# Performance work log

Measured on AMD Instinct MI355X. Metric: run time of the kernel, lower is better.

The kernel has to match this reference:

```python
import jax, jax.numpy as jnp
from jax import lax
import numpy as np

B, T, A = 128, 2048, 3
H = 100  # LSTM units
F = 64   # conv filters


def setup_inputs() -> dict:
    key = jax.random.key(0)
    ks = jax.random.split(key, 8)
    s = lambda k, shape, scale: (jax.random.normal(k, shape, dtype=jnp.float32) * scale)
    return {
        "state_input": s(ks[0], (B, T, 1), 1.0),
        "conv_w": s(ks[1], (2, 1, F), 0.5),
        "conv_b": jnp.zeros((F,), jnp.float32),
        "lstm1_w": s(ks[2], (F, 4 * H), 0.08),
        "lstm1_u": s(ks[3], (H, 4 * H), 0.08),
        "lstm1_b": jnp.zeros((4 * H,), jnp.float32),
        "lstm2_w": s(ks[4], (H, 4 * H), 0.08),
        "lstm2_u": s(ks[5], (H, 4 * H), 0.08),
        "lstm2_b": jnp.zeros((4 * H,), jnp.float32),
        "dense_w": s(ks[6], (H, A), 0.1),
        "dense_b": jnp.zeros((A,), jnp.float32),
    }


def _lstm_relu(x, W, U, b, return_sequences):
    # Keras LSTM with activation='relu', recurrent_activation='sigmoid'.
    # Gate order: i, f, g(candidate), o. h = o * relu(c).
    Bz = x.shape[0]
    xz = jnp.einsum("btf,fg->btg", x, W) + b  # precompute input projections [B,T,4H]
    h0 = jnp.zeros((Bz, U.shape[0]), x.dtype)
    c0 = jnp.zeros_like(h0)

    def step(carry, xz_t):
        h, c = carry
        z = xz_t + h @ U
        i, f, g, o = jnp.split(z, 4, axis=-1)
        i = jax.nn.sigmoid(i)
        f = jax.nn.sigmoid(f)
        g = jax.nn.relu(g)
        o = jax.nn.sigmoid(o)
        c = f * c + i * g
        h = o * jax.nn.relu(c)
        return (h, c), (h if return_sequences else 0.0)

    (h_last, _), hs = lax.scan(step, (h0, c0), jnp.swapaxes(xz, 0, 1))
    if return_sequences:
        return jnp.swapaxes(hs, 0, 1)  # [B,T,H]
    return h_last


def reference(state_input, conv_w, conv_b, lstm1_w, lstm1_u, lstm1_b,
              lstm2_w, lstm2_u, lstm2_b, dense_w, dense_b):
    # Conv1D(filters=64, kernel_size=2, padding='valid', relu): [B,T,1]->[B,T-1,64]
    x = lax.conv_general_dilated(
        state_input, conv_w, window_strides=(1,), padding="VALID",
        dimension_numbers=("NWC", "WIO", "NWC"))
    x = jax.nn.relu(x + conv_b)
    # MaxPool1D(pool_size=1) is the identity.
    x = _lstm_relu(x, lstm1_w, lstm1_u, lstm1_b, return_sequences=True)
    # Dropout at inference is identity.
    x = _lstm_relu(x, lstm2_w, lstm2_u, lstm2_b, return_sequences=False)  # [B,H]
    logits = x @ dense_w + dense_b
    return jax.nn.softmax(logits, axis=-1)
```

## Files before the change

### kernel.cpp

```cpp
#include <hip/hip_runtime.h>
#include <math.h>


typedef _Float16 h2 __attribute__((ext_vector_type(2)));

#define TT 2048
#define TP 2047
#define HH 100
#define G4 400
#define FF 64
#define NB 128

#define X1R 176
#define CBQ 104
#define NPW (400 * 88)
#define NCW (400 * 100)
#define CHK 64
#define NCHUNK 32
#define RINGC 4
#define CHUNK_DW (CHK * 50)

#define WS_FLAGS (NPW + NCW)
#define WS_RING  (WS_FLAGS + 256)

#define FD2(w, xs, acc) acc = __builtin_amdgcn_fdot2(w, xs, acc, false)
#define B2(f) __builtin_bit_cast(h2, f)

static __device__ __forceinline__ float psum2(float z) {
    int p = __builtin_amdgcn_update_dpp(0, __builtin_bit_cast(int, z),
                                        0xB1, 0xF, 0xF, true);
    return z + __builtin_bit_cast(float, p);
}
static __device__ __forceinline__ float xswap2(float z) {
    int p = __builtin_amdgcn_update_dpp(0, __builtin_bit_cast(int, z),
                                        0x4E, 0xF, 0xF, true);
    return __builtin_bit_cast(float, p);
}
static __device__ __forceinline__ float sig(float z) {
    return 1.0f / (1.0f + __expf(-z));
}
static __device__ __forceinline__ void step_barrier() {
    __builtin_amdgcn_sched_barrier(0);
    asm volatile("s_waitcnt lgkmcnt(0)" ::: "memory");
    __builtin_amdgcn_sched_barrier(0);
    __builtin_amdgcn_s_barrier();
    __builtin_amdgcn_sched_barrier(0);
}

__global__ void prep_weights(const float* __restrict__ w1, const float* __restrict__ u1,
                             const float* __restrict__ w2, const float* __restrict__ u2,
                             h2* __restrict__ ws)
{
    const int idx = blockIdx.x * 256 + threadIdx.x;
    if (idx >= NPW + NCW) return;
    float lo = 0.f, hi = 0.f;
    if (idx < NPW) {
        const int rt = idx / 88, r = idx % 88;
        const int qq = (r >> 2) * 2 + ((r & 3) >> 1);
        const int gs = r & 1;
        const int p = rt >> 2, g2 = (rt >> 1) & 1, kh = rt & 1;
        const int col = (2 * g2 + gs) * HH + p;
        const int E0 = 2 * qq;
#pragma unroll
        for (int e = 0; e < 2; ++e) {
            const int E = E0 + e;
            float v = 0.f;
            if (E < 82) {
                const int k = kh * 82 + E;
                v = (k < FF) ? w1[k * G4 + col] : u1[(k - FF) * G4 + col];
            }
            if (e == 0) lo = v; else hi = v;
        }
    } else {
        const int i2 = idx - NPW;
        const int rt = i2 / 100, r = i2 % 100;
        const int qq = (r >> 2) * 2 + ((r & 3) >> 1);
        const int gs = r & 1;
        const int p = rt >> 2, g2 = (rt >> 1) & 1, kh = rt & 1;
        const int col = (2 * g2 + gs) * HH + p;
        const int k0 = 2 * qq;
        const float* M = kh ? u2 : w2;
        lo = M[k0 * G4 + col];
        hi = M[(k0 + 1) * G4 + col];
    }
    ws[idx] = h2{(_Float16)lo, (_Float16)hi};
}

__global__ __launch_bounds__(448, 1)
void fused_lstm_kernel(const float* __restrict__ s,
                       const float* __restrict__ conv_w,
                       const float* __restrict__ conv_b,
                       const float* __restrict__ b1,
                       const float* __restrict__ b2,
                       const float* __restrict__ dw, const float* __restrict__ db,
                       h2* __restrict__ wpk,
                       float* __restrict__ out)
{
    const int tid  = threadIdx.x;
    const int bb   = blockIdx.x;
    const int b    = bb & (NB - 1);
    const bool prod = bb < NB;

    int* pflag = (int*)(wpk + WS_FLAGS) + b;
    int* aflag = (int*)(wpk + WS_FLAGS) + 128 + b;
    unsigned* ring = (unsigned*)(wpk + WS_RING) + (size_t)b * (RINGC * CHUNK_DW);

    __shared__ float s_buf[TT];
    __shared__ __align__(16) _Float16 X1[2 * X1R];
    __shared__ __align__(16) _Float16 CB[CHK * CBQ];
    __shared__ __align__(16) _Float16 HR[2 * CBQ];

    if (prod) {
        for (int i = tid; i < TT; i += 448) s_buf[i] = s[(size_t)b * TT + i];
        if (tid < X1R) ((unsigned*)X1)[tid] = 0u;
    } else {
        if (tid < CBQ) ((unsigned*)HR)[tid] = 0u;
        if (tid < CHK * 2)
            ((unsigned*)CB)[(tid >> 1) * 52 + 50 + (tid & 1)] = 0u;
    }
    __syncthreads();

    if (prod) {
        const int rt = tid;
        const int active = rt < 400;
        const int lrt = active ? rt : 0;
        const int p  = lrt >> 2;
        const int g2 = (lrt >> 1) & 1;
        const int kh = lrt & 1;
        const int cL = (2 * g2) * HH + p;

        h2 wa[44], wb[44];
        {
            const float4* w4 = (const float4*)(wpk + (size_t)lrt * 88);
#pragma unroll
            for (int j = 0; j < 22; ++j) {
                const float4 v = w4[j];
                wa[2*j]   = B2(v.x); wb[2*j]   = B2(v.y);
                wa[2*j+1] = B2(v.z); wb[2*j+1] = B2(v.w);
            }
        }
        const float bL = b1[cL], bH = b1[cL + HH];
        const int hoff = (p < 18) ? (64 + p) : (p + 70);

        const int f1 = rt - 400;
        float cv0 = 0.f, cv1 = 0.f, cb0 = 0.f, cv0b = 0.f, cv1b = 0.f, cb0b = 0.f;
        if (!active) {
            cv0 = conv_w[f1]; cv1 = conv_w[FF + f1]; cb0 = conv_b[f1];
            if (f1 < 16) { cv0b = conv_w[48 + f1]; cv1b = conv_w[FF + 48 + f1]; cb0b = conv_b[48 + f1]; }
        }
        if (!active) {
            X1[f1] = (_Float16)fmaxf(fmaf(s_buf[0], cv0, fmaf(s_buf[1], cv1, cb0)), 0.f);
            if (f1 < 16)
                X1[48 + f1] = (_Float16)fmaxf(fmaf(s_buf[0], cv0b, fmaf(s_buf[1], cv1b, cb0b)), 0.f);
        }
        __syncthreads();

        float c = 0.0f;
        for (int t = 0; t < TP; ++t) {
            if ((t & 63) == 0) {
                const int k = t >> 6;
                if (tid == 0 && k >= RINGC) {
                    int g = 0;
                    while (__hip_atomic_load(aflag, __ATOMIC_ACQUIRE,
                                             __HIP_MEMORY_SCOPE_AGENT) < k - (RINGC - 1)
                           && g < 50000000) { ++g; __builtin_amdgcn_s_sleep(8); }
                }
                __syncthreads();
            }
            if (active) {
                _Float16* cur = X1 + (t & 1) * X1R;
                _Float16* nx1 = X1 + ((t & 1) ^ 1) * X1R;
                float za0 = 0.f, za1 = 0.f, zb0 = 0.f, zb1 = 0.f;
                const float4* vb = (const float4*)(cur + kh * 88);
#pragma unroll
                for (int r2 = 0; r2 < 11; ++r2) {
                    const float4 v = vb[r2];
                    FD2(wa[4*r2+0], B2(v.x), za0); FD2(wb[4*r2+0], B2(v.x), zb0);
                    FD2(wa[4*r2+1], B2(v.y), za1); FD2(wb[4*r2+1], B2(v.y), zb1);
                    FD2(wa[4*r2+2], B2(v.z), za0); FD2(wb[4*r2+2], B2(v.z), zb0);
                    FD2(wa[4*r2+3], B2(v.w), za1); FD2(wb[4*r2+3], B2(v.w), zb1);
                }
                const float zaS = psum2(za0 + za1) + bL;
                const float zbS = psum2(zb0 + zb1) + bH;
                const float oa = xswap2(zaS), ob = xswap2(zbS);
                const float zi = g2 ? oa  : zaS;
                const float zf = g2 ? ob  : zbS;
                const float zg = g2 ? zaS : oa;
                const float zo = g2 ? zbS : ob;
                c = fmaf(sig(zf), c, sig(zi) * fmaxf(zg, 0.f));
                const float h = sig(zo) * fmaxf(c, 0.f);
                if ((rt & 3) == 0) {
                    const _Float16 hq = (_Float16)h;
                    nx1[hoff] = hq;
                    const unsigned hb = (unsigned)__builtin_bit_cast(unsigned short, hq);
                    const unsigned prt =
                        (unsigned)__builtin_amdgcn_ds_swizzle((int)hb, 0x101F) & 0xFFFFu;
                    if (!(p & 1))
                        __hip_atomic_store(ring + ((t >> 6) & 3) * CHUNK_DW
                                                + (t & 63) * 50 + (p >> 1),
                                           hb | (prt << 16), __ATOMIC_RELAXED,
                                           __HIP_MEMORY_SCOPE_AGENT);
                }
                if (((t & 63) == 63) || (t == TP - 1))
                    asm volatile("s_waitcnt vmcnt(0)" ::: "memory");
            } else if (t + 1 < TP) {
                _Float16* nx1 = X1 + ((t & 1) ^ 1) * X1R;
                nx1[f1] = (_Float16)fmaxf(
                    fmaf(s_buf[t + 1], cv0, fmaf(s_buf[t + 2], cv1, cb0)), 0.f);
                if (f1 < 16)
                    nx1[48 + f1] = (_Float16)fmaxf(
                        fmaf(s_buf[t + 1], cv0b, fmaf(s_buf[t + 2], cv1b, cb0b)), 0.f);
            }
            step_barrier();
            if (tid == 0 && (((t & 63) == 63) || (t == TP - 1)))
                __hip_atomic_fetch_add(pflag, 1, __ATOMIC_RELEASE,
                                       __HIP_MEMORY_SCOPE_AGENT);
        }
    } else {
        const int rt = tid;
        const int active = rt < 400;
        const int lrt = active ? rt : 0;
        const int p  = lrt >> 2;
        const int g2 = (lrt >> 1) & 1;
        const int kh = lrt & 1;
        const int cL = (2 * g2) * HH + p;

        h2 wa[50], wb[50];
        {
            const float4* w4 = (const float4*)(wpk + NPW + (size_t)lrt * 100);
#pragma unroll
            for (int j = 0; j < 25; ++j) {
                const float4 v = w4[j];
                wa[2*j]   = B2(v.x); wb[2*j]   = B2(v.y);
                wa[2*j+1] = B2(v.z); wb[2*j+1] = B2(v.w);
            }
        }
        const float bL = b2[cL], bH = b2[cL + HH];
        __syncthreads();

        float c = 0.0f;
        for (int k = 0; k < NCHUNK; ++k) {
            if (tid == 0) {
                int g = 0;
                while (__hip_atomic_load(pflag, __ATOMIC_ACQUIRE,
                                         __HIP_MEMORY_SCOPE_AGENT) < k + 1
                       && g < 50000000) { ++g; __builtin_amdgcn_s_sleep(8); }
            }
            __syncthreads();
            const int csz = (TP - (k << 6) < CHK) ? (TP - (k << 6)) : CHK;
            unsigned* gsrc = ring + (k & 3) * CHUNK_DW;
            for (int d = tid; d < csz * 50; d += 448)
                ((unsigned*)CB)[(d / 50) * 52 + (d % 50)] =
                    __hip_atomic_load(gsrc + d, __ATOMIC_RELAXED,
                                      __HIP_MEMORY_SCOPE_AGENT);
            __syncthreads();
            if (tid == 0)
                __hip_atomic_fetch_add(aflag, 1, __ATOMIC_RELAXED,
                                       __HIP_MEMORY_SCOPE_AGENT);
            for (int lt = 0; lt < csz; ++lt) {
                const int t = (k << 6) + lt;
                if (active) {
                    const _Float16* base = kh ? (HR + (t & 1) * CBQ)
                                              : (CB + lt * CBQ);
                    float za0 = 0.f, za1 = 0.f, zb0 = 0.f, zb1 = 0.f;
                    const float4* vb = (const float4*)base;
#pragma unroll
                    for (int r2 = 0; r2 < 12; ++r2) {
                        const float4 v = vb[r2];
                        FD2(wa[4*r2+0], B2(v.x), za0); FD2(wb[4*r2+0], B2(v.x), zb0);
                        FD2(wa[4*r2+1], B2(v.y), za1); FD2(wb[4*r2+1], B2(v.y), zb1);
                        FD2(wa[4*r2+2], B2(v.z), za0); FD2(wb[4*r2+2], B2(v.z), zb0);
                        FD2(wa[4*r2+3], B2(v.w), za1); FD2(wb[4*r2+3], B2(v.w), zb1);
                    }
                    {
                        const float2 tv = *(const float2*)(base + 96);
                        FD2(wa[48], B2(tv.x), za0); FD2(wb[48], B2(tv.x), zb0);
                        FD2(wa[49], B2(tv.y), za1); FD2(wb[49], B2(tv.y), zb1);
                    }
                    const float zaS = psum2(za0 + za1) + bL;
                    const float zbS = psum2(zb0 + zb1) + bH;
                    const float oa = xswap2(zaS), ob = xswap2(zbS);
                    const float zi = g2 ? oa  : zaS;
                    const float zf = g2 ? ob  : zbS;
                    const float zg = g2 ? zaS : oa;
                    const float zo = g2 ? zbS : ob;
                    c = fmaf(sig(zf), c, sig(zi) * fmaxf(zg, 0.f));
                    const float h = sig(zo) * fmaxf(c, 0.f);
                    if ((rt & 3) == 0)
                        HR[((t & 1) ^ 1) * CBQ + p] = (_Float16)h;
                }
                step_barrier();
            }
        }

        if (rt == 0) {
            float l[3];
#pragma unroll
            for (int a = 0; a < 3; ++a) {
                float acc = db[a];
                for (int j = 0; j < HH; ++j)
                    acc = fmaf((float)HR[CBQ + j], dw[j * 3 + a], acc);
                l[a] = acc;
            }
            const float m = fmaxf(l[0], fmaxf(l[1], l[2]));
            const float e0 = __expf(l[0] - m), e1 = __expf(l[1] - m), e2 = __expf(l[2] - m);
            const float inv = 1.0f / (e0 + e1 + e2);
            out[b * 3 + 0] = e0 * inv;
            out[b * 3 + 1] = e1 * inv;
            out[b * 3 + 2] = e2 * inv;
        }
    }
}

extern "C" void kernel_launch(void* const* d_in, const int* in_sizes, int n_in,
                              void* d_out, int out_size, void* d_ws, size_t ws_size,
                              hipStream_t stream) {
    const float* s      = (const float*)d_in[0];
    const float* conv_w = (const float*)d_in[1];
    const float* conv_b = (const float*)d_in[2];
    const float* w1     = (const float*)d_in[3];
    const float* u1     = (const float*)d_in[4];
    const float* b1     = (const float*)d_in[5];
    const float* w2     = (const float*)d_in[6];
    const float* u2     = (const float*)d_in[7];
    const float* b2     = (const float*)d_in[8];
    const float* dw     = (const float*)d_in[9];
    const float* db     = (const float*)d_in[10];

    h2* ws = (h2*)d_ws;
    hipMemsetAsync((void*)((int*)(ws + WS_FLAGS)), 0, 256 * sizeof(int), stream);
    const int nh2 = NPW + NCW;
    prep_weights<<<(nh2 + 255) / 256, 256, 0, stream>>>(w1, u1, w2, u2, ws);
    fused_lstm_kernel<<<256, 448, 0, stream>>>(
        s, conv_w, conv_b, b1, b2, dw, db, ws, (float*)d_out);
}
```

Measured before the change: 2.063 ms.

## Halve threads per LSTM step by dropping the K-split reduction across lane pairs

Each gate pair is now computed by one thread over the full input dimension instead of being split across two threads, which removes the DPP pair-sum and reduces the block from 448 to 256 threads. Weights are repacked so each thread holds twice as many fp16 pairs in registers, and the conv lanes, h placement and swizzle pattern are adjusted to match. The aim is fewer waves per block and a cheaper cross-lane step on the serial recurrence, in exchange for a longer dependent dot-product chain and more register pressure per thread.

New measurement: 2.156 ms. 4.5% more time.

```diff
diff --git a/kernel.cpp b/kernel.cpp
--- a/kernel.cpp
+++ b/kernel.cpp
@@ -11,10 +11,10 @@
 #define FF 64
 #define NB 128
 
-#define X1R 176
+#define X1R 168
 #define CBQ 104
-#define NPW (400 * 88)
-#define NCW (400 * 100)
+#define NPW (200 * 164)
+#define NCW (200 * 200)
 #define CHK 64
 #define NCHUNK 32
 #define RINGC 4
@@ -26,14 +26,9 @@
 #define FD2(w, xs, acc) acc = __builtin_amdgcn_fdot2(w, xs, acc, false)
 #define B2(f) __builtin_bit_cast(h2, f)
 
-static __device__ __forceinline__ float psum2(float z) {
+static __device__ __forceinline__ float xswap1(float z) {
     int p = __builtin_amdgcn_update_dpp(0, __builtin_bit_cast(int, z),
                                         0xB1, 0xF, 0xF, true);
-    return z + __builtin_bit_cast(float, p);
-}
-static __device__ __forceinline__ float xswap2(float z) {
-    int p = __builtin_amdgcn_update_dpp(0, __builtin_bit_cast(int, z),
-                                        0x4E, 0xF, 0xF, true);
     return __builtin_bit_cast(float, p);
 }
 static __device__ __forceinline__ float sig(float z) {
@@ -55,38 +50,72 @@
     if (idx >= NPW + NCW) return;
     float lo = 0.f, hi = 0.f;
     if (idx < NPW) {
-        const int rt = idx / 88, r = idx % 88;
+        const int rt = idx / 164, r = idx % 164;
         const int qq = (r >> 2) * 2 + ((r & 3) >> 1);
         const int gs = r & 1;
-        const int p = rt >> 2, g2 = (rt >> 1) & 1, kh = rt & 1;
+        const int p = rt >> 1, g2 = rt & 1;
         const int col = (2 * g2 + gs) * HH + p;
-        const int E0 = 2 * qq;
+        const int k0 = 2 * qq;
 #pragma unroll
         for (int e = 0; e < 2; ++e) {
-            const int E = E0 + e;
-            float v = 0.f;
-            if (E < 82) {
-                const int k = kh * 82 + E;
-                v = (k < FF) ? w1[k * G4 + col] : u1[(k - FF) * G4 + col];
-            }
+            const int k = k0 + e;
+            const float v = (k < FF) ? w1[k * G4 + col] : u1[(k - FF) * G4 + col];
             if (e == 0) lo = v; else hi = v;
         }
     } else {
         const int i2 = idx - NPW;
-        const int rt = i2 / 100, r = i2 % 100;
+        const int rt = i2 / 200, r = i2 % 200;
         const int qq = (r >> 2) * 2 + ((r & 3) >> 1);
         const int gs = r & 1;
-        const int p = rt >> 2, g2 = (rt >> 1) & 1, kh = rt & 1;
+        const int p = rt >> 1, g2 = rt & 1;
         const int col = (2 * g2 + gs) * HH + p;
         const int k0 = 2 * qq;
-        const float* M = kh ? u2 : w2;
-        lo = M[k0 * G4 + col];
-        hi = M[(k0 + 1) * G4 + col];
+#pragma unroll
+        for (int e = 0; e < 2; ++e) {
+            const int k = k0 + e;
+            const float v = (k < HH) ? w2[k * G4 + col] : u2[(k - HH) * G4 + col];
+            if (e == 0) lo = v; else hi = v;
+        }
     }
     ws[idx] = h2{(_Float16)lo, (_Float16)hi};
 }
 
-__global__ __launch_bounds__(448, 1)
+#define PDOTF(base) { const float4* vb = (const float4*)(base); \
+_Pragma("unroll") \
+    for (int r2 = 0; r2 < 20; ++r2) { \
+        const float4 v = vb[r2]; \
+        FD2(wa[4*r2+0], B2(v.x), za0); FD2(wb[4*r2+0], B2(v.x), zb0); \
+        FD2(wa[4*r2+1], B2(v.y), za1); FD2(wb[4*r2+1], B2(v.y), zb1); \
+        FD2(wa[4*r2+2], B2(v.z), za0); FD2(wb[4*r2+2], B2(v.z), zb0); \
+        FD2(wa[4*r2+3], B2(v.w), za1); FD2(wb[4*r2+3], B2(v.w), zb1); \
+    } \
+    { const float2 tv = *(const float2*)((base) + 160); \
+      FD2(wa[80], B2(tv.x), za0); FD2(wb[80], B2(tv.x), zb0); \
+      FD2(wa[81], B2(tv.y), za1); FD2(wb[81], B2(tv.y), zb1); } }
+
+#define CDOTH(base, WO) { const float4* vb = (const float4*)(base); \
+_Pragma("unroll") \
+    for (int r2 = 0; r2 < 12; ++r2) { \
+        const float4 v = vb[r2]; \
+        FD2(wa[(WO)+4*r2+0], B2(v.x), za0); FD2(wb[(WO)+4*r2+0], B2(v.x), zb0); \
+        FD2(wa[(WO)+4*r2+1], B2(v.y), za1); FD2(wb[(WO)+4*r2+1], B2(v.y), zb1); \
+        FD2(wa[(WO)+4*r2+2], B2(v.z), za0); FD2(wb[(WO)+4*r2+2], B2(v.z), zb0); \
+        FD2(wa[(WO)+4*r2+3], B2(v.w), za1); FD2(wb[(WO)+4*r2+3], B2(v.w), zb1); \
+    } \
+    { const float2 tv = *(const float2*)((base) + 96); \
+      FD2(wa[(WO)+48], B2(tv.x), za0); FD2(wb[(WO)+48], B2(tv.x), zb0); \
+      FD2(wa[(WO)+49], B2(tv.y), za1); FD2(wb[(WO)+49], B2(tv.y), zb1); } }
+
+#define GCELL1(zaS, zbS, cc, hh_) { \
+    const float oa = xswap1(zaS), ob = xswap1(zbS); \
+    const float zi = g2 ? oa  : zaS; \
+    const float zf = g2 ? ob  : zbS; \
+    const float zg = g2 ? zaS : oa; \
+    const float zo = g2 ? zbS : ob; \
+    cc = fmaf(sig(zf), cc, sig(zi) * fmaxf(zg, 0.f)); \
+    hh_ = sig(zo) * fmaxf(cc, 0.f); }
+
+__global__ __launch_bounds__(256, 1)
 void fused_lstm_kernel(const float* __restrict__ s,
                        const float* __restrict__ conv_w,
                        const float* __restrict__ conv_b,
@@ -111,7 +140,7 @@
     __shared__ __align__(16) _Float16 HR[2 * CBQ];
 
     if (prod) {
-        for (int i = tid; i < TT; i += 448) s_buf[i] = s[(size_t)b * TT + i];
+        for (int i = tid; i < TT; i += 256) s_buf[i] = s[(size_t)b * TT + i];
         if (tid < X1R) ((unsigned*)X1)[tid] = 0u;
     } else {
         if (tid < CBQ) ((unsigned*)HR)[tid] = 0u;
@@ -122,36 +151,34 @@
 
     if (prod) {
         const int rt = tid;
-        const int active = rt < 400;
+        const int active = rt < 200;
         const int lrt = active ? rt : 0;
-        const int p  = lrt >> 2;
-        const int g2 = (lrt >> 1) & 1;
-        const int kh = lrt & 1;
+        const int p  = lrt >> 1;
+        const int g2 = lrt & 1;
         const int cL = (2 * g2) * HH + p;
 
-        h2 wa[44], wb[44];
+        h2 wa[82], wb[82];
         {
-            const float4* w4 = (const float4*)(wpk + (size_t)lrt * 88);
-#pragma unroll
-            for (int j = 0; j < 22; ++j) {
+            const float4* w4 = (const float4*)(wpk + (size_t)lrt * 164);
+#pragma unroll
+            for (int j = 0; j < 41; ++j) {
                 const float4 v = w4[j];
                 wa[2*j]   = B2(v.x); wb[2*j]   = B2(v.y);
                 wa[2*j+1] = B2(v.z); wb[2*j+1] = B2(v.w);
             }
         }
         const float bL = b1[cL], bH = b1[cL + HH];
-        const int hoff = (p < 18) ? (64 + p) : (p + 70);
-
-        const int f1 = rt - 400;
+
+        const int f1 = rt - 200;
         float cv0 = 0.f, cv1 = 0.f, cb0 = 0.f, cv0b = 0.f, cv1b = 0.f, cb0b = 0.f;
         if (!active) {
             cv0 = conv_w[f1]; cv1 = conv_w[FF + f1]; cb0 = conv_b[f1];
-            if (f1 < 16) { cv0b = conv_w[48 + f1]; cv1b = conv_w[FF + 48 + f1]; cb0b = conv_b[48 + f1]; }
+            if (f1 < 8) { cv0b = conv_w[56 + f1]; cv1b = conv_w[FF + 56 + f1]; cb0b = conv_b[56 + f1]; }
         }
         if (!active) {
             X1[f1] = (_Float16)fmaxf(fmaf(s_buf[0], cv0, fmaf(s_buf[1], cv1, cb0)), 0.f);
-            if (f1 < 16)
-                X1[48 + f1] = (_Float16)fmaxf(fmaf(s_buf[0], cv0b, fmaf(s_buf[1], cv1b, cb0b)), 0.f);
+            if (f1 < 8)
+                X1[56 + f1] = (_Float16)fmaxf(fmaf(s_buf[0], cv0b, fmaf(s_buf[1], cv1b, cb0b)), 0.f);
         }
         __syncthreads();
 
@@ -171,30 +198,17 @@
                 _Float16* cur = X1 + (t & 1) * X1R;
                 _Float16* nx1 = X1 + ((t & 1) ^ 1) * X1R;
                 float za0 = 0.f, za1 = 0.f, zb0 = 0.f, zb1 = 0.f;
-                const float4* vb = (const float4*)(cur + kh * 88);
-#pragma unroll
-                for (int r2 = 0; r2 < 11; ++r2) {
-                    const float4 v = vb[r2];
-                    FD2(wa[4*r2+0], B2(v.x), za0); FD2(wb[4*r2+0], B2(v.x), zb0);
-                    FD2(wa[4*r2+1], B2(v.y), za1); FD2(wb[4*r2+1], B2(v.y), zb1);
-                    FD2(wa[4*r2+2], B2(v.z), za0); FD2(wb[4*r2+2], B2(v.z), zb0);
-                    FD2(wa[4*r2+3], B2(v.w), za1); FD2(wb[4*r2+3], B2(v.w), zb1);
-                }
-                const float zaS = psum2(za0 + za1) + bL;
-                const float zbS = psum2(zb0 + zb1) + bH;
-                const float oa = xswap2(zaS), ob = xswap2(zbS);
-                const float zi = g2 ? oa  : zaS;
-                const float zf = g2 ? ob  : zbS;
-                const float zg = g2 ? zaS : oa;
-                const float zo = g2 ? zbS : ob;
-                c = fmaf(sig(zf), c, sig(zi) * fmaxf(zg, 0.f));
-                const float h = sig(zo) * fmaxf(c, 0.f);
-                if ((rt & 3) == 0) {
+                PDOTF(cur)
+                const float zaS = za0 + za1 + bL;
+                const float zbS = zb0 + zb1 + bH;
+                float h;
+                GCELL1(zaS, zbS, c, h)
+                if (!g2) {
                     const _Float16 hq = (_Float16)h;
-                    nx1[hoff] = hq;
+                    nx1[FF + p] = hq;
                     const unsigned hb = (unsigned)__builtin_bit_cast(unsigned short, hq);
                     const unsigned prt =
-                        (unsigned)__builtin_amdgcn_ds_swizzle((int)hb, 0x101F) & 0xFFFFu;
+                        (unsigned)__builtin_amdgcn_ds_swizzle((int)hb, 0x081F) & 0xFFFFu;
                     if (!(p & 1))
                         __hip_atomic_store(ring + ((t >> 6) & 3) * CHUNK_DW
                                                 + (t & 63) * 50 + (p >> 1),
@@ -207,8 +221,8 @@
                 _Float16* nx1 = X1 + ((t & 1) ^ 1) * X1R;
                 nx1[f1] = (_Float16)fmaxf(
                     fmaf(s_buf[t + 1], cv0, fmaf(s_buf[t + 2], cv1, cb0)), 0.f);
-                if (f1 < 16)
-                    nx1[48 + f1] = (_Float16)fmaxf(
+                if (f1 < 8)
+                    nx1[56 + f1] = (_Float16)fmaxf(
                         fmaf(s_buf[t + 1], cv0b, fmaf(s_buf[t + 2], cv1b, cb0b)), 0.f);
             }
             step_barrier();
@@ -218,18 +232,17 @@
         }
     } else {
         const int rt = tid;
-        const int active = rt < 400;
+        const int active = rt < 200;
         const int lrt = active ? rt : 0;
-        const int p  = lrt >> 2;
-        const int g2 = (lrt >> 1) & 1;
-        const int kh = lrt & 1;
+        const int p  = lrt >> 1;
+        const int g2 = lrt & 1;
         const int cL = (2 * g2) * HH + p;
 
-        h2 wa[50], wb[50];
+        h2 wa[100], wb[100];
         {
-            const float4* w4 = (const float4*)(wpk + NPW + (size_t)lrt * 100);
-#pragma unroll
-            for (int j = 0; j < 25; ++j) {
+            const float4* w4 = (const float4*)(wpk + NPW + (size_t)lrt * 200);
+#pragma unroll
+            for (int j = 0; j < 50; ++j) {
                 const float4 v = w4[j];
                 wa[2*j]   = B2(v.x); wb[2*j]   = B2(v.y);
                 wa[2*j+1] = B2(v.z); wb[2*j+1] = B2(v.w);
@@ -249,7 +262,7 @@
             __syncthreads();
             const int csz = (TP - (k << 6) < CHK) ? (TP - (k << 6)) : CHK;
             unsigned* gsrc = ring + (k & 3) * CHUNK_DW;
-            for (int d = tid; d < csz * 50; d += 448)
+            for (int d = tid; d < csz * 50; d += 256)
                 ((unsigned*)CB)[(d / 50) * 52 + (d % 50)] =
                     __hip_atomic_load(gsrc + d, __ATOMIC_RELAXED,
                                       __HIP_MEMORY_SCOPE_AGENT);
@@ -260,33 +273,14 @@
             for (int lt = 0; lt < csz; ++lt) {
                 const int t = (k << 6) + lt;
                 if (active) {
-                    const _Float16* base = kh ? (HR + (t & 1) * CBQ)
-                                              : (CB + lt * CBQ);
                     float za0 = 0.f, za1 = 0.f, zb0 = 0.f, zb1 = 0.f;
-                    const float4* vb = (const float4*)base;
-#pragma unroll
-                    for (int r2 = 0; r2 < 12; ++r2) {
-                        const float4 v = vb[r2];
-                        FD2(wa[4*r2+0], B2(v.x), za0); FD2(wb[4*r2+0], B2(v.x), zb0);
-                        FD2(wa[4*r2+1], B2(v.y), za1); FD2(wb[4*r2+1], B2(v.y), zb1);
-                        FD2(wa[4*r2+2], B2(v.z), za0); FD2(wb[4*r2+2], B2(v.z), zb0);
-                        FD2(wa[4*r2+3], B2(v.w), za1); FD2(wb[4*r2+3], B2(v.w), zb1);
-                    }
-                    {
-                        const float2 tv = *(const float2*)(base + 96);
-                        FD2(wa[48], B2(tv.x), za0); FD2(wb[48], B2(tv.x), zb0);
-                        FD2(wa[49], B2(tv.y), za1); FD2(wb[49], B2(tv.y), zb1);
-                    }
-                    const float zaS = psum2(za0 + za1) + bL;
-                    const float zbS = psum2(zb0 + zb1) + bH;
-                    const float oa = xswap2(zaS), ob = xswap2(zbS);
-                    const float zi = g2 ? oa  : zaS;
-                    const float zf = g2 ? ob  : zbS;
-                    const float zg = g2 ? zaS : oa;
-                    const float zo = g2 ? zbS : ob;
-                    c = fmaf(sig(zf), c, sig(zi) * fmaxf(zg, 0.f));
-                    const float h = sig(zo) * fmaxf(c, 0.f);
-                    if ((rt & 3) == 0)
+                    CDOTH(CB + lt * CBQ, 0)
+                    CDOTH(HR + (t & 1) * CBQ, 50)
+                    const float zaS = za0 + za1 + bL;
+                    const float zbS = zb0 + zb1 + bH;
+                    float h;
+                    GCELL1(zaS, zbS, c, h)
+                    if (!g2)
                         HR[((t & 1) ^ 1) * CBQ + p] = (_Float16)h;
                 }
                 step_barrier();
@@ -331,6 +325,6 @@
     hipMemsetAsync((void*)((int*)(ws + WS_FLAGS)), 0, 256 * sizeof(int), stream);
     const int nh2 = NPW + NCW;
     prep_weights<<<(nh2 + 255) / 256, 256, 0, stream>>>(w1, u1, w2, u2, ws);
-    fused_lstm_kernel<<<256, 448, 0, stream>>>(
+    fused_lstm_kernel<<<256, 256, 0, stream>>>(
         s, conv_w, conv_b, b1, b2, dw, db, ws, (float*)d_out);
 }
```
